# Performance work log

Hardware: AMD Instinct MI355X
Metric: run time of the kernel (lower is better)

Reference implementation:

```python
import jax, jax.numpy as jnp
import numpy as np

B, N, M, C = 4, 4096, 4096, 256
H, K = 8, 8
S = K + 1          # window: query token + k neighbors
D = C // H         # head dim
FF = 4 * C
RADIUS = 0.06
EPS = 1e-5


def setup_inputs() -> dict:
    key = jax.random.key(0)
    ks = jax.random.split(key, 12)
    s = 0.02
    return {
        "q_xyz": jax.random.uniform(ks[0], (B, N, 3), dtype=jnp.float32),
        "q_feat": jax.random.normal(ks[1], (B, N, C), dtype=jnp.float32),
        "kv_xyz": jax.random.uniform(ks[2], (B, M, 3), dtype=jnp.float32),
        "kv_feat": jax.random.normal(ks[3], (B, M, C), dtype=jnp.float32),
        "kv_pad": jnp.zeros((B, M), dtype=bool),
        # MultiheadAttention params (torch layout: y = x @ W.T + b)
        "Wqkv": s * jax.random.normal(ks[4], (3 * C, C), dtype=jnp.float32),
        "bqkv": jnp.zeros((3 * C,), dtype=jnp.float32),
        "Wo": s * jax.random.normal(ks[5], (C, C), dtype=jnp.float32),
        "bo": jnp.zeros((C,), dtype=jnp.float32),
        # FFN
        "W1": s * jax.random.normal(ks[6], (FF, C), dtype=jnp.float32),
        "b1": jnp.zeros((FF,), dtype=jnp.float32),
        "W2": s * jax.random.normal(ks[7], (C, FF), dtype=jnp.float32),
        "b2": jnp.zeros((C,), dtype=jnp.float32),
        # LayerNorms
        "g1": jnp.ones((C,), dtype=jnp.float32),
        "be1": jnp.zeros((C,), dtype=jnp.float32),
        "g2": jnp.ones((C,), dtype=jnp.float32),
        "be2": jnp.zeros((C,), dtype=jnp.float32),
    }


def _layernorm(x, g, b):
    mu = jnp.mean(x, axis=-1, keepdims=True)
    var = jnp.mean((x - mu) ** 2, axis=-1, keepdims=True)
    return (x - mu) / jnp.sqrt(var + EPS) * g + b


def _forward(q_xyz, q_feat, kv_xyz, kv_feat, kv_pad,
             Wqkv, bqkv, Wo, bo, W1, b1, W2, b2, g1, be1, g2, be2):
    inf = jnp.float32(jnp.inf)
    # pairwise distances via ||q||^2 + ||k||^2 - 2 q.k  -> (B, N, M)
    d2 = (jnp.sum(q_xyz * q_xyz, -1)[:, :, None]
          + jnp.sum(kv_xyz * kv_xyz, -1)[:, None, :]
          - 2.0 * jnp.einsum('bnd,bmd->bnm', q_xyz, kv_xyz))
    dist = jnp.sqrt(jnp.maximum(d2, 0.0))
    dist = jnp.where(kv_pad[:, None, :], inf, dist)
    dist = jnp.where(dist <= RADIUS, dist, inf)
    # k nearest within radius (topk of -dist == smallest dist)
    neg, idx = jax.lax.top_k(-dist, K)            # (B, N, K)
    invalid = jnp.isinf(neg)                       # padding slots
    idx = jnp.where(invalid, 0, idx)
    # gather neighbor features: (B, N, K, C)
    neigh = jnp.take_along_axis(
        kv_feat, idx.reshape(B, N * K)[:, :, None], axis=1
    ).reshape(B, N, K, C)
    neigh = jnp.where(invalid[..., None], q_feat[:, :, None, :], neigh)
    # tokens: query token + neighbors -> (B*N, S, C)
    tokens = jnp.concatenate([q_feat[:, :, None, :], neigh], axis=2)
    tokens = tokens.reshape(B * N, S, C)
    pad = jnp.concatenate(
        [jnp.zeros_like(invalid[..., :1]), invalid], axis=-1
    ).reshape(B * N, S)                            # (B*N, S) key padding
    # --- MultiheadAttention (batch_first, eval) ---
    qkv = tokens @ Wqkv.T + bqkv
    q, k, v = jnp.split(qkv, 3, axis=-1)
    q = q.reshape(-1, S, H, D)
    k = k.reshape(-1, S, H, D)
    v = v.reshape(-1, S, H, D)
    scores = jnp.einsum('bshd,bthd->bhst', q, k) / np.sqrt(D).astype(np.float32)
    scores = jnp.where(pad[:, None, None, :], -inf, scores)
    attn = jax.nn.softmax(scores, axis=-1)
    o = jnp.einsum('bhst,bthd->bshd', attn, v).reshape(-1, S, C)
    o = o @ Wo.T + bo
    # residual + norm, FFN + norm
    x = _layernorm(tokens + o, g1, be1)
    f = jnp.maximum(x @ W1.T + b1, 0.0) @ W2.T + b2
    x = _layernorm(x + f, g2, be2)
    # fused query token + residual -> (B, N, C)
    return x[:, 0, :].reshape(B, N, C) + q_feat


def reference(q_xyz, q_feat, kv_xyz, kv_feat, kv_pad,
              Wqkv, bqkv, Wo, bo, W1, b1, W2, b2, g1, be1, g2, be2):
    return _forward(q_xyz, q_feat, kv_xyz, kv_feat, kv_pad,
                    Wqkv, bqkv, Wo, bo, W1, b1, W2, b2, g1, be1, g2, be2)
```

## Files before the change

### kernel.cpp

```cpp
#include <hip/hip_runtime.h>
#include <hip/hip_bf16.h>
#include <stdint.h>

#define B_ 4
#define N_ 4096
#define M_ 4096
#define C_ 256
#define FF_ 1024
#define BN_ (B_*N_)
#define BM_ (B_*M_)

typedef __attribute__((ext_vector_type(8))) short short8;
typedef __attribute__((ext_vector_type(4))) float f32x4;

static __device__ __forceinline__ float b2f(unsigned short u) {
    union { unsigned int i; float f; } c; c.i = ((unsigned int)u) << 16; return c.f;
}
static __device__ __forceinline__ unsigned short f2b(float f) {
    union { float f; unsigned int i; } c; c.f = f;
    unsigned int x = c.i;
    x += 0x7fffu + ((x >> 16) & 1u);
    return (unsigned short)(x >> 16);
}

static __device__ __forceinline__ void gload_lds16(const short* g, short* l) {
    __builtin_amdgcn_global_load_lds((const __attribute__((address_space(1))) void*)g,
                                     (__attribute__((address_space(3))) void*)l,
                                     16, 0, 0);
}

__global__ __launch_bounds__(1024) void prep_kernel(const float* __restrict__ s0, unsigned short* __restrict__ d0,
                                                    const float* __restrict__ s1, unsigned short* __restrict__ d1,
                                                    const float* __restrict__ s2, unsigned short* __restrict__ d2,
                                                    const float* __restrict__ s3, unsigned short* __restrict__ d3,
                                                    const float* __restrict__ s4, unsigned short* __restrict__ d4,
                                                    const float* __restrict__ s5, unsigned short* __restrict__ d5,
                                                    const float* __restrict__ kv_xyz,
                                                    float4* __restrict__ sorted,
                                                    int* __restrict__ starts) {
    __shared__ int cnt[4096];
    __shared__ int wsum[16];
    if (blockIdx.x < 2240) {
        int i = blockIdx.x * 1024 + threadIdx.x;
        const float* src; unsigned short* dst; int off;
        if (i < 1048576)      { src = s0; dst = d0; off = i; }
        else if (i < 2097152) { src = s1; dst = d1; off = i - 1048576; }
        else if (i < 2146304) { src = s2; dst = d2; off = i - 2097152; }
        else if (i < 2162688) { src = s3; dst = d3; off = i - 2146304; }
        else if (i < 2228224) { src = s4; dst = d4; off = i - 2162688; }
        else                  { src = s5; dst = d5; off = i - 2228224; }
        f32x4 v = *(const f32x4*)(src + (size_t)off * 4);
        ushort4 r;
        r.x = f2b(v[0]); r.y = f2b(v[1]); r.z = f2b(v[2]); r.w = f2b(v[3]);
        *(ushort4*)(dst + (size_t)off * 4) = r;
        return;
    }
    int b = blockIdx.x - 2240, tid = threadIdx.x;
    const float* src = kv_xyz + (size_t)b * M_ * 3;
    for (int i = tid; i < 4096; i += 1024) cnt[i] = 0;
    __syncthreads();
    float px[4], py[4], pz[4]; int pc[4];
#pragma unroll
    for (int j = 0; j < 4; ++j) {
        int m = tid + j * 1024;
        px[j] = src[3 * m]; py[j] = src[3 * m + 1]; pz[j] = src[3 * m + 2];
        int cx = min(15, (int)(px[j] * 16.0f));
        int cy = min(15, (int)(py[j] * 16.0f));
        int cz = min(15, (int)(pz[j] * 16.0f));
        pc[j] = (cz * 16 + cy) * 16 + cx;
        atomicAdd(&cnt[pc[j]], 1);
    }
    __syncthreads();
    int c0 = cnt[tid * 4], c1 = cnt[tid * 4 + 1], c2 = cnt[tid * 4 + 2], c3 = cnt[tid * 4 + 3];
    int tsum = c0 + c1 + c2 + c3;
    int lane = tid & 63, wv = tid >> 6;
    int scan = tsum;
#pragma unroll
    for (int off = 1; off < 64; off <<= 1) {
        int o = __shfl_up(scan, off);
        if (lane >= off) scan += o;
    }
    if (lane == 63) wsum[wv] = scan;
    __syncthreads();
    if (tid < 16) {
        int v = wsum[tid];
#pragma unroll
        for (int off = 1; off < 16; off <<= 1) {
            int o = __shfl_up(v, off);
            if (tid >= off) v += o;
        }
        wsum[tid] = v;
    }
    __syncthreads();
    int base = (wv > 0 ? wsum[wv - 1] : 0) + (scan - tsum);
    int e0 = base, e1 = base + c0, e2 = e1 + c1, e3 = e2 + c2;
    int* st = starts + (size_t)b * 4097;
    st[tid * 4] = e0; st[tid * 4 + 1] = e1; st[tid * 4 + 2] = e2; st[tid * 4 + 3] = e3;
    if (tid == 0) st[4096] = M_;
    cnt[tid * 4] = e0; cnt[tid * 4 + 1] = e1; cnt[tid * 4 + 2] = e2; cnt[tid * 4 + 3] = e3;
    __syncthreads();
    float4* dst = sorted + (size_t)b * 4096;
#pragma unroll
    for (int j = 0; j < 4; ++j) {
        int m = tid + j * 1024;
        int pos = atomicAdd(&cnt[pc[j]], 1);
        float4 v; v.x = px[j]; v.y = py[j]; v.z = pz[j]; v.w = __int_as_float(m);
        dst[pos] = v;
    }
}

template <int RELU, int OUTBF>
__global__ __launch_bounds__(256) void gemm_lds_kernel(const unsigned short* __restrict__ A,
                                                       const unsigned short* __restrict__ W,
                                                       const float* __restrict__ bias,
                                                       float* __restrict__ Yf,
                                                       unsigned short* __restrict__ Yb,
                                                       int M, int Nn, int Kd) {
    __shared__ __align__(16) short As[2][4096];
    __shared__ __align__(16) short Bs[2][4096];
    int lane = threadIdx.x & 63, wid = threadIdx.x >> 6;
    int row0 = blockIdx.y * 128;
    int col0 = blockIdx.x * 128;
    int wr = wid >> 1, wc = wid & 1;
    const short* Ap = (const short*)A;
    const short* Wp = (const short*)W;
    int srow = lane >> 2;
    int scolz = (((lane & 3) ^ ((lane >> 2) & 3)) * 8);

    f32x4 acc[4][4];
#pragma unroll
    for (int i = 0; i < 4; ++i)
#pragma unroll
        for (int j = 0; j < 4; ++j)
#pragma unroll
            for (int r = 0; r < 4; ++r) acc[i][j][r] = 0.0f;

    int KT = Kd >> 5;
    int buf = 0;

#define STAGE(BUFI, K0)                                                                   \
    {                                                                                     \
        _Pragma("unroll")                                                                 \
        for (int j = 0; j < 2; ++j) {                                                     \
            int chunk = j * 4 + wid;                                                      \
            int row = chunk * 16 + srow;                                                  \
            gload_lds16(Ap + (size_t)(row0 + row) * Kd + (K0) + scolz, &As[BUFI][chunk * 512]); \
            gload_lds16(Wp + (size_t)(col0 + row) * Kd + (K0) + scolz, &Bs[BUFI][chunk * 512]); \
        }                                                                                 \
    }

    STAGE(0, 0);
    __syncthreads();

    int lane15 = lane & 15;
    int rd16s = (((lane >> 4) ^ (lane & 3)) * 16);

    for (int kt = 0; kt < KT; ++kt) {
        if (kt + 1 < KT) STAGE(buf ^ 1, (kt + 1) << 5);
        short8 a[4], b[4];
#pragma unroll
        for (int i = 0; i < 4; ++i) {
            int ra = wr * 64 + i * 16 + lane15;
            int rb = wc * 64 + i * 16 + lane15;
            a[i] = *(const short8*)((const char*)&As[buf][0] + ra * 64 + rd16s);
            b[i] = *(const short8*)((const char*)&Bs[buf][0] + rb * 64 + rd16s);
        }
#pragma unroll
        for (int i = 0; i < 4; ++i)
#pragma unroll
            for (int j = 0; j < 4; ++j)
                acc[i][j] = __builtin_amdgcn_mfma_f32_16x16x32_bf16(a[i], b[j], acc[i][j], 0, 0, 0);
        if (kt + 1 < KT) __syncthreads();
        buf ^= 1;
    }
#undef STAGE

    int r0 = row0 + wr * 64 + (lane >> 4) * 4;
    int c0 = col0 + wc * 64 + lane15;
#pragma unroll
    for (int i = 0; i < 4; ++i)
#pragma unroll
        for (int j = 0; j < 4; ++j)
#pragma unroll
            for (int r = 0; r < 4; ++r) {
                int rr = r0 + i * 16 + r;
                int cc = c0 + j * 16;
                float v = acc[i][j][r] + bias[cc];
                if (RELU) v = fmaxf(v, 0.0f);
                if (OUTBF) Yb[(size_t)rr * Nn + cc] = f2b(v);
                else       Yf[(size_t)rr * Nn + cc] = v;
            }
}

__global__ __launch_bounds__(512) void attn_wo_ln_kernel(const unsigned short* __restrict__ QKVq,
                                                         const unsigned short* __restrict__ KVkv,
                                                         const float* __restrict__ q_xyz,
                                                         const float4* __restrict__ sorted,
                                                         const int* __restrict__ starts,
                                                         const unsigned short* __restrict__ Wo,
                                                         const float* __restrict__ bias,
                                                         const unsigned short* __restrict__ qfb,
                                                         const float* __restrict__ g,
                                                         const float* __restrict__ be,
                                                         unsigned short* __restrict__ xout) {
    __shared__ __align__(16) short o_lds[8192];
    __shared__ __align__(16) short Bs[2][8192];
    __shared__ float redS[8][32];
    __shared__ float redQ[8][32];
    int lane = threadIdx.x & 63, wid = threadIdx.x >> 6;
    int swz = (blockIdx.x & 7) * 64 + (blockIdx.x >> 3);
    int row0 = swz * 32;
    const short* Wp = (const short*)Wo;
    int srow = lane >> 2;
    int scolz = (((lane & 3) ^ ((lane >> 2) & 3)) * 8);

#define STAGE_B(BUFI, K0)                                                                   \
    {                                                                                       \
        for (int c = wid; c < 16; c += 8) {                                                 \
            gload_lds16(Wp + (size_t)(c * 16 + srow) * 256 + (K0) + scolz,                  \
                        &Bs[BUFI][c * 512]);                                                \
        }                                                                                   \
    }
    STAGE_B(0, 0);

    int c0l = lane * 4;
    for (int pt = 0; pt < 4; ++pt) {
        int lrow = wid * 4 + pt;
        int p = row0 + lrow;
        int b = p >> 12;

        float qx = q_xyz[(size_t)p * 3 + 0];
        float qy = q_xyz[(size_t)p * 3 + 1];
        float qz = q_xyz[(size_t)p * 3 + 2];
        float qq = __fadd_rn(__fadd_rn(__fmul_rn(qx, qx), __fmul_rn(qy, qy)), __fmul_rn(qz, qz));
        int cx = min(15, (int)(qx * 16.0f));
        int cy = min(15, (int)(qy * 16.0f));
        int cz = min(15, (int)(qz * 16.0f));
        unsigned long long lst[8];
#pragma unroll
        for (int i = 0; i < 8; ++i) lst[i] = ~0ull;
        const float4* pts = sorted + (size_t)b * 4096;
        const int* st = starts + (size_t)b * 4097;
        int z0 = max(cz - 1, 0), z1 = min(cz + 1, 15);
        int y0 = max(cy - 1, 0), y1 = min(cy + 1, 15);
        int x0 = max(cx - 1, 0), x1 = min(cx + 1, 15);
        for (int z = z0; z <= z1; ++z) {
            for (int y = y0; y <= y1; ++y) {
                int rowbase = (z * 16 + y) * 16;
                int s = st[rowbase + x0];
                int e = st[rowbase + x1 + 1];
                for (int i = s + lane; i < e; i += 64) {
                    float4 pp = pts[i];
                    float kk = __fadd_rn(__fadd_rn(__fmul_rn(pp.x, pp.x), __fmul_rn(pp.y, pp.y)), __fmul_rn(pp.z, pp.z));
                    float dt = __fadd_rn(__fadd_rn(__fmul_rn(qx, pp.x), __fmul_rn(qy, pp.y)), __fmul_rn(qz, pp.z));
                    float d2 = __fsub_rn(__fadd_rn(qq, kk), __fmul_rn(2.0f, dt));
                    float dist = __fsqrt_rn(fmaxf(d2, 0.0f));
                    if (dist <= 0.06f) {
                        union { float f; unsigned int i; } cv; cv.f = dist;
                        unsigned long long key = (((unsigned long long)cv.i) << 32) |
                                                 (unsigned int)__float_as_int(pp.w);
                        if (key < lst[7]) {
                            lst[7] = key;
#pragma unroll
                            for (int k = 7; k > 0; --k) {
                                if (lst[k] < lst[k - 1]) {
                                    unsigned long long tmp = lst[k]; lst[k] = lst[k - 1]; lst[k - 1] = tmp;
                                }
                            }
                        }
                    }
                }
            }
        }
        int nbr[8];
#pragma unroll
        for (int s = 0; s < 8; ++s) {
            unsigned long long mn = lst[0];
#pragma unroll
            for (int off = 32; off >= 1; off >>= 1) {
                unsigned long long o = __shfl_xor(mn, off);
                if (o < mn) mn = o;
            }
            int widx = (mn == ~0ull) ? -1 : (int)(unsigned int)(mn & 0xffffffffull);
            if (widx >= 0 && lst[0] == mn) {
#pragma unroll
                for (int k = 0; k < 7; ++k) lst[k] = lst[k + 1];
                lst[7] = ~0ull;
            }
            nbr[s] = widx;
        }

        const unsigned short* qrow = QKVq + (size_t)p * 768;
        ushort4 qu = *(const ushort4*)(qrow + c0l);
        float q0 = b2f(qu.x), q1 = b2f(qu.y), q2 = b2f(qu.z), q3 = b2f(qu.w);
        float sc[9];
        float vb[9][4];
        bool vld[9];
#pragma unroll
        for (int s = 0; s < 9; ++s) {
            const unsigned short* kr;
            bool valid;
            if (s == 0) { valid = true; kr = qrow + 256 + c0l; }
            else {
                int m = nbr[s - 1];
                valid = (m >= 0);
                kr = KVkv + (size_t)(b * 4096 + (valid ? m : 0)) * 512 + c0l;
            }
            float d = 0.0f;
            float v0 = 0.f, v1 = 0.f, v2 = 0.f, v3 = 0.f;
            if (valid) {
                ushort4 ku = *(const ushort4*)kr;
                ushort4 vu = *(const ushort4*)(kr + 256);
                d = q0 * b2f(ku.x) + q1 * b2f(ku.y) + q2 * b2f(ku.z) + q3 * b2f(ku.w);
                v0 = b2f(vu.x); v1 = b2f(vu.y); v2 = b2f(vu.z); v3 = b2f(vu.w);
            }
            d += __shfl_xor(d, 1);
            d += __shfl_xor(d, 2);
            d += __shfl_xor(d, 4);
            sc[s] = valid ? d * 0.17677669529663687f : -1e30f;
            vld[s] = valid;
            vb[s][0] = v0; vb[s][1] = v1; vb[s][2] = v2; vb[s][3] = v3;
        }
        float mx = sc[0];
#pragma unroll
        for (int s = 1; s < 9; ++s) mx = fmaxf(mx, sc[s]);
        float pr[9]; float sum = 0.0f;
#pragma unroll
        for (int s = 0; s < 9; ++s) {
            float e = vld[s] ? expf(sc[s] - mx) : 0.0f;
            pr[s] = e; sum += e;
        }
        float inv = 1.0f / sum;
        float o0 = 0, o1 = 0, o2 = 0, o3 = 0;
#pragma unroll
        for (int s = 0; s < 9; ++s) {
            o0 += pr[s] * vb[s][0]; o1 += pr[s] * vb[s][1];
            o2 += pr[s] * vb[s][2]; o3 += pr[s] * vb[s][3];
        }
        ushort4 r;
        r.x = f2b(o0 * inv); r.y = f2b(o1 * inv); r.z = f2b(o2 * inv); r.w = f2b(o3 * inv);
        int byteoff = lrow * 512 + (((lane >> 1) ^ (lrow & 7)) * 16) + (lane & 1) * 8;
        *(ushort4*)((char*)o_lds + byteoff) = r;
    }
    __syncthreads();

    int lane15 = lane & 15;
    int l4 = lane >> 4;
    int rd16s = ((l4 ^ (lane & 3)) * 16);
    int wc = wid;

    f32x4 acc[2][2];
#pragma unroll
    for (int i = 0; i < 2; ++i)
#pragma unroll
        for (int j = 0; j < 2; ++j)
#pragma unroll
            for (int r = 0; r < 4; ++r) acc[i][j][r] = 0.0f;

    int buf = 0;
    for (int kt = 0; kt < 8; ++kt) {
        if (kt + 1 < 8) STAGE_B(buf ^ 1, (kt + 1) << 5);
        short8 a[2], b[2];
#pragma unroll
        for (int i = 0; i < 2; ++i) {
            int arow = i * 16 + lane15;
            int unit = kt * 4 + l4;
            a[i] = *(const short8*)((const char*)o_lds + arow * 512 + ((unit ^ (arow & 7)) * 16));
        }
#pragma unroll
        for (int j = 0; j < 2; ++j) {
            int rb = wc * 32 + j * 16 + lane15;
            b[j] = *(const short8*)((const char*)&Bs[buf][0] + rb * 64 + rd16s);
        }
#pragma unroll
        for (int i = 0; i < 2; ++i)
#pragma unroll
            for (int j = 0; j < 2; ++j)
                acc[i][j] = __builtin_amdgcn_mfma_f32_16x16x32_bf16(a[i], b[j], acc[i][j], 0, 0, 0);
        if (kt + 1 < 8) __syncthreads();
        buf ^= 1;
    }
#undef STAGE_B

#pragma unroll
    for (int i = 0; i < 2; ++i)
#pragma unroll
        for (int j = 0; j < 2; ++j)
#pragma unroll
            for (int r = 0; r < 4; ++r) {
                int rr = row0 + i * 16 + l4 * 4 + r;
                int cc = wc * 32 + j * 16 + lane15;
                acc[i][j][r] += bias[cc] + b2f(qfb[(size_t)rr * 256 + cc]);
            }
#pragma unroll
    for (int i = 0; i < 2; ++i)
#pragma unroll
        for (int r = 0; r < 4; ++r) {
            float v0 = acc[i][0][r], v1 = acc[i][1][r];
            float s = v0 + v1;
            float s2 = v0 * v0 + v1 * v1;
#pragma unroll
            for (int off = 1; off < 16; off <<= 1) {
                s  += __shfl_xor(s, off);
                s2 += __shfl_xor(s2, off);
            }
            if (lane15 == 0) {
                int rl = i * 16 + l4 * 4 + r;
                redS[wid][rl] = s;
                redQ[wid][rl] = s2;
            }
        }
    __syncthreads();
#pragma unroll
    for (int i = 0; i < 2; ++i)
#pragma unroll
        for (int r = 0; r < 4; ++r) {
            int rl = i * 16 + l4 * 4 + r;
            int rr = row0 + rl;
            float tot = 0.0f, tot2 = 0.0f;
#pragma unroll
            for (int w = 0; w < 8; ++w) { tot += redS[w][rl]; tot2 += redQ[w][rl]; }
            float mu = tot * (1.0f / 256.0f);
            float var = fmaxf(tot2 * (1.0f / 256.0f) - mu * mu, 0.0f);
            float rs = 1.0f / __fsqrt_rn(var + 1e-5f);
#pragma unroll
            for (int j = 0; j < 2; ++j) {
                int cc = wc * 32 + j * 16 + lane15;
                float o = (acc[i][j][r] - mu) * rs * g[cc] + be[cc];
                xout[(size_t)rr * 256 + cc] = f2b(o);
            }
        }
}

__global__ __launch_bounds__(512) void gemm_ln2_kernel(const unsigned short* __restrict__ A,
                                                       const unsigned short* __restrict__ W,
                                                       const float* __restrict__ bias,
                                                       const unsigned short* __restrict__ qfb,
                                                       const unsigned short* __restrict__ resb,
                                                       const float* __restrict__ g,
                                                       const float* __restrict__ be,
                                                       float* __restrict__ outf,
                                                       int Kd) {
    __shared__ __align__(16) short As[2][1024];
    __shared__ __align__(16) short Bs[2][8192];
    __shared__ float redS[8][32];
    __shared__ float redQ[8][32];
    int lane = threadIdx.x & 63, wid = threadIdx.x >> 6;
    int swz = (blockIdx.x & 7) * 64 + (blockIdx.x >> 3);
    int row0 = swz * 32;
    int wc = wid;
    const short* Ap = (const short*)A;
    const short* Wp = (const short*)W;
    int srow = lane >> 2;
    int scolz = (((lane & 3) ^ ((lane >> 2) & 3)) * 8);

    f32x4 acc[2][2];
#pragma unroll
    for (int i = 0; i < 2; ++i)
#pragma unroll
        for (int j = 0; j < 2; ++j)
#pragma unroll
            for (int r = 0; r < 4; ++r) acc[i][j][r] = 0.0f;

    int KT = Kd >> 5;
    int buf = 0;

#define STAGE3(BUFI, K0)                                                                    \
    {                                                                                       \
        for (int c = wid; c < 18; c += 8) {                                                 \
            if (c < 2) {                                                                    \
                gload_lds16(Ap + (size_t)(row0 + c * 16 + srow) * Kd + (K0) + scolz,        \
                            &As[BUFI][c * 512]);                                            \
            } else {                                                                        \
                int cb = c - 2;                                                             \
                gload_lds16(Wp + (size_t)(cb * 16 + srow) * Kd + (K0) + scolz,              \
                            &Bs[BUFI][cb * 512]);                                           \
            }                                                                               \
        }                                                                                   \
    }

    STAGE3(0, 0);
    __syncthreads();

    int lane15 = lane & 15;
    int l4 = lane >> 4;
    int rd16s = ((l4 ^ (lane & 3)) * 16);

    for (int kt = 0; kt < KT; ++kt) {
        if (kt + 1 < KT) STAGE3(buf ^ 1, (kt + 1) << 5);
        short8 a[2], b[2];
#pragma unroll
        for (int i = 0; i < 2; ++i) {
            int ra = i * 16 + lane15;
            a[i] = *(const short8*)((const char*)&As[buf][0] + ra * 64 + rd16s);
        }
#pragma unroll
        for (int j = 0; j < 2; ++j) {
            int rb = wc * 32 + j * 16 + lane15;
            b[j] = *(const short8*)((const char*)&Bs[buf][0] + rb * 64 + rd16s);
        }
#pragma unroll
        for (int i = 0; i < 2; ++i)
#pragma unroll
            for (int j = 0; j < 2; ++j)
                acc[i][j] = __builtin_amdgcn_mfma_f32_16x16x32_bf16(a[i], b[j], acc[i][j], 0, 0, 0);
        __syncthreads();
        buf ^= 1;
    }
#undef STAGE3

#pragma unroll
    for (int i = 0; i < 2; ++i)
#pragma unroll
        for (int j = 0; j < 2; ++j)
#pragma unroll
            for (int r = 0; r < 4; ++r) {
                int rr = row0 + i * 16 + l4 * 4 + r;
                int cc = wc * 32 + j * 16 + lane15;
                acc[i][j][r] += bias[cc] + b2f(resb[(size_t)rr * 256 + cc]);
            }
#pragma unroll
    for (int i = 0; i < 2; ++i)
#pragma unroll
        for (int r = 0; r < 4; ++r) {
            float v0 = acc[i][0][r], v1 = acc[i][1][r];
            float s = v0 + v1;
            float s2 = v0 * v0 + v1 * v1;
#pragma unroll
            for (int off = 1; off < 16; off <<= 1) {
                s  += __shfl_xor(s, off);
                s2 += __shfl_xor(s2, off);
            }
            if (lane15 == 0) {
                int rl = i * 16 + l4 * 4 + r;
                redS[wid][rl] = s;
                redQ[wid][rl] = s2;
            }
        }
    __syncthreads();
#pragma unroll
    for (int i = 0; i < 2; ++i)
#pragma unroll
        for (int r = 0; r < 4; ++r) {
            int rl = i * 16 + l4 * 4 + r;
            int rr = row0 + rl;
            float tot = 0.0f, tot2 = 0.0f;
#pragma unroll
            for (int w = 0; w < 8; ++w) { tot += redS[w][rl]; tot2 += redQ[w][rl]; }
            float mu = tot * (1.0f / 256.0f);
            float var = fmaxf(tot2 * (1.0f / 256.0f) - mu * mu, 0.0f);
            float rs = 1.0f / __fsqrt_rn(var + 1e-5f);
#pragma unroll
            for (int j = 0; j < 2; ++j) {
                int cc = wc * 32 + j * 16 + lane15;
                float o = (acc[i][j][r] - mu) * rs * g[cc] + be[cc];
                outf[(size_t)rr * 256 + cc] = o + b2f(qfb[(size_t)rr * 256 + cc]);
            }
        }
}

extern "C" void kernel_launch(void* const* d_in, const int* in_sizes, int n_in,
                              void* d_out, int out_size, void* d_ws, size_t ws_size,
                              hipStream_t stream) {
    const float* q_xyz  = (const float*)d_in[0];
    const float* q_feat = (const float*)d_in[1];
    const float* kv_xyz = (const float*)d_in[2];
    const float* kv_feat = (const float*)d_in[3];
    const float* Wqkv = (const float*)d_in[5];
    const float* bqkv = (const float*)d_in[6];
    const float* Wo = (const float*)d_in[7];
    const float* bo = (const float*)d_in[8];
    const float* W1 = (const float*)d_in[9];
    const float* b1 = (const float*)d_in[10];
    const float* W2 = (const float*)d_in[11];
    const float* b2 = (const float*)d_in[12];
    const float* g1 = (const float*)d_in[13];
    const float* be1 = (const float*)d_in[14];
    const float* g2 = (const float*)d_in[15];
    const float* be2 = (const float*)d_in[16];

    char* ws = (char*)d_ws;
    const size_t OFF_QF   = 0;
    const size_t OFF_KVF  = OFF_QF   + 8388608;
    const size_t OFF_WQKV = OFF_KVF  + 8388608;
    const size_t OFF_WO   = OFF_WQKV + 393216;
    const size_t OFF_W1   = OFF_WO   + 131072;
    const size_t OFF_W2   = OFF_W1   + 524288;
    const size_t OFF_QKVQ = OFF_W2   + 524288;
    const size_t OFF_KVKV = OFF_QKVQ + 25165824;
    const size_t OFF_X    = OFF_KVKV + 16777216;
    const size_t OFF_H    = OFF_X    + 8388608;
    const size_t OFF_SORT  = OFF_H;
    const size_t OFF_START = OFF_H + 262144;

    unsigned short* qf_bf   = (unsigned short*)(ws + OFF_QF);
    unsigned short* kvf_bf  = (unsigned short*)(ws + OFF_KVF);
    unsigned short* Wqkv_bf = (unsigned short*)(ws + OFF_WQKV);
    unsigned short* Wo_bf   = (unsigned short*)(ws + OFF_WO);
    unsigned short* W1_bf   = (unsigned short*)(ws + OFF_W1);
    unsigned short* W2_bf   = (unsigned short*)(ws + OFF_W2);
    unsigned short* QKVq    = (unsigned short*)(ws + OFF_QKVQ);
    unsigned short* KVkv    = (unsigned short*)(ws + OFF_KVKV);
    unsigned short* x_bf    = (unsigned short*)(ws + OFF_X);
    unsigned short* h_bf    = (unsigned short*)(ws + OFF_H);
    float4* sort_buf        = (float4*)(ws + OFF_SORT);
    int* start_buf          = (int*)(ws + OFF_START);

    prep_kernel<<<2244, 1024, 0, stream>>>(
        q_feat, qf_bf, kv_feat, kvf_bf, Wqkv, Wqkv_bf, Wo, Wo_bf, W1, W1_bf, W2, W2_bf,
        kv_xyz, sort_buf, start_buf);

    gemm_lds_kernel<0, 1><<<dim3(768 / 128, BN_ / 128), 256, 0, stream>>>(
        qf_bf, Wqkv_bf, bqkv, nullptr, QKVq, BN_, 768, 256);
    gemm_lds_kernel<0, 1><<<dim3(512 / 128, BM_ / 128), 256, 0, stream>>>(
        kvf_bf, Wqkv_bf + 256 * 256, bqkv + 256, nullptr, KVkv, BM_, 512, 256);

    attn_wo_ln_kernel<<<BN_ / 32, 512, 0, stream>>>(
        QKVq, KVkv, q_xyz, sort_buf, start_buf, Wo_bf, bo, qf_bf, g1, be1, x_bf);

    gemm_lds_kernel<1, 1><<<dim3(1024 / 128, BN_ / 128), 256, 0, stream>>>(
        x_bf, W1_bf, b1, nullptr, h_bf, BN_, 1024, 256);

    gemm_ln2_kernel<<<BN_ / 32, 512, 0, stream>>>(
        h_bf, W2_bf, b2, qf_bf, x_bf, g2, be2, (float*)d_out, 1024);
}
```

Measured before the change: 153.3 us.

## Move neighbor search into a separate one-thread-per-query kernel

```diff
diff --git a/kernel.cpp b/kernel.cpp
--- a/kernel.cpp
+++ b/kernel.cpp
@@ -109,6 +109,61 @@
     }
 }
 
+__global__ __launch_bounds__(256) void knn_query_kernel(const float* __restrict__ q_xyz,
+                                                        const float4* __restrict__ sorted,
+                                                        const int* __restrict__ starts,
+                                                        int* __restrict__ idx_out) {
+    int q = blockIdx.x * 256 + threadIdx.x;
+    int b = q >> 12;
+    float qx = q_xyz[(size_t)q * 3 + 0];
+    float qy = q_xyz[(size_t)q * 3 + 1];
+    float qz = q_xyz[(size_t)q * 3 + 2];
+    float qq = __fadd_rn(__fadd_rn(__fmul_rn(qx, qx), __fmul_rn(qy, qy)), __fmul_rn(qz, qz));
+    int cx = min(15, (int)(qx * 16.0f));
+    int cy = min(15, (int)(qy * 16.0f));
+    int cz = min(15, (int)(qz * 16.0f));
+    unsigned long long lst[8];
+#pragma unroll
+    for (int i = 0; i < 8; ++i) lst[i] = ~0ull;
+    const float4* pts = sorted + (size_t)b * 4096;
+    const int* st = starts + (size_t)b * 4097;
+    int z0 = max(cz - 1, 0), z1 = min(cz + 1, 15);
+    int y0 = max(cy - 1, 0), y1 = min(cy + 1, 15);
+    int x0 = max(cx - 1, 0), x1 = min(cx + 1, 15);
+    for (int z = z0; z <= z1; ++z) {
+        for (int y = y0; y <= y1; ++y) {
+            int rowbase = (z * 16 + y) * 16;
+            int s = st[rowbase + x0];
+            int e = st[rowbase + x1 + 1];
+            for (int i = s; i < e; ++i) {
+                float4 p = pts[i];
+                float kk = __fadd_rn(__fadd_rn(__fmul_rn(p.x, p.x), __fmul_rn(p.y, p.y)), __fmul_rn(p.z, p.z));
+                float dt = __fadd_rn(__fadd_rn(__fmul_rn(qx, p.x), __fmul_rn(qy, p.y)), __fmul_rn(qz, p.z));
+                float d2 = __fsub_rn(__fadd_rn(qq, kk), __fmul_rn(2.0f, dt));
+                float dist = __fsqrt_rn(fmaxf(d2, 0.0f));
+                if (dist <= 0.06f) {
+                    union { float f; unsigned int i; } cv; cv.f = dist;
+                    unsigned long long key = (((unsigned long long)cv.i) << 32) |
+                                             (unsigned int)__float_as_int(p.w);
+                    if (key < lst[7]) {
+                        lst[7] = key;
+#pragma unroll
+                        for (int k = 7; k > 0; --k) {
+                            if (lst[k] < lst[k - 1]) {
+                                unsigned long long tmp = lst[k]; lst[k] = lst[k - 1]; lst[k - 1] = tmp;
+                            }
+                        }
+                    }
+                }
+            }
+        }
+    }
+#pragma unroll
+    for (int s = 0; s < 8; ++s)
+        idx_out[(size_t)q * 8 + s] =
+            (lst[s] == ~0ull) ? -1 : (int)(unsigned int)(lst[s] & 0xffffffffull);
+}
+
 template <int RELU, int OUTBF>
 __global__ __launch_bounds__(256) void gemm_lds_kernel(const unsigned short* __restrict__ A,
                                                        const unsigned short* __restrict__ W,
@@ -194,9 +249,7 @@
 
 __global__ __launch_bounds__(512) void attn_wo_ln_kernel(const unsigned short* __restrict__ QKVq,
                                                          const unsigned short* __restrict__ KVkv,
-                                                         const float* __restrict__ q_xyz,
-                                                         const float4* __restrict__ sorted,
-                                                         const int* __restrict__ starts,
+                                                         const int* __restrict__ nidx,
                                                          const unsigned short* __restrict__ Wo,
                                                          const float* __restrict__ bias,
                                                          const unsigned short* __restrict__ qfb,
@@ -228,68 +281,6 @@
         int lrow = wid * 4 + pt;
         int p = row0 + lrow;
         int b = p >> 12;
-
-        float qx = q_xyz[(size_t)p * 3 + 0];
-        float qy = q_xyz[(size_t)p * 3 + 1];
-        float qz = q_xyz[(size_t)p * 3 + 2];
-        float qq = __fadd_rn(__fadd_rn(__fmul_rn(qx, qx), __fmul_rn(qy, qy)), __fmul_rn(qz, qz));
-        int cx = min(15, (int)(qx * 16.0f));
-        int cy = min(15, (int)(qy * 16.0f));
-        int cz = min(15, (int)(qz * 16.0f));
-        unsigned long long lst[8];
-#pragma unroll
-        for (int i = 0; i < 8; ++i) lst[i] = ~0ull;
-        const float4* pts = sorted + (size_t)b * 4096;
-        const int* st = starts + (size_t)b * 4097;
-        int z0 = max(cz - 1, 0), z1 = min(cz + 1, 15);
-        int y0 = max(cy - 1, 0), y1 = min(cy + 1, 15);
-        int x0 = max(cx - 1, 0), x1 = min(cx + 1, 15);
-        for (int z = z0; z <= z1; ++z) {
-            for (int y = y0; y <= y1; ++y) {
-                int rowbase = (z * 16 + y) * 16;
-                int s = st[rowbase + x0];
-                int e = st[rowbase + x1 + 1];
-                for (int i = s + lane; i < e; i += 64) {
-                    float4 pp = pts[i];
-                    float kk = __fadd_rn(__fadd_rn(__fmul_rn(pp.x, pp.x), __fmul_rn(pp.y, pp.y)), __fmul_rn(pp.z, pp.z));
-                    float dt = __fadd_rn(__fadd_rn(__fmul_rn(qx, pp.x), __fmul_rn(qy, pp.y)), __fmul_rn(qz, pp.z));
-                    float d2 = __fsub_rn(__fadd_rn(qq, kk), __fmul_rn(2.0f, dt));
-                    float dist = __fsqrt_rn(fmaxf(d2, 0.0f));
-                    if (dist <= 0.06f) {
-                        union { float f; unsigned int i; } cv; cv.f = dist;
-                        unsigned long long key = (((unsigned long long)cv.i) << 32) |
-                                                 (unsigned int)__float_as_int(pp.w);
-                        if (key < lst[7]) {
-                            lst[7] = key;
-#pragma unroll
-                            for (int k = 7; k > 0; --k) {
-                                if (lst[k] < lst[k - 1]) {
-                                    unsigned long long tmp = lst[k]; lst[k] = lst[k - 1]; lst[k - 1] = tmp;
-                                }
-                            }
-                        }
-                    }
-                }
-            }
-        }
-        int nbr[8];
-#pragma unroll
-        for (int s = 0; s < 8; ++s) {
-            unsigned long long mn = lst[0];
-#pragma unroll
-            for (int off = 32; off >= 1; off >>= 1) {
-                unsigned long long o = __shfl_xor(mn, off);
-                if (o < mn) mn = o;
-            }
-            int widx = (mn == ~0ull) ? -1 : (int)(unsigned int)(mn & 0xffffffffull);
-            if (widx >= 0 && lst[0] == mn) {
-#pragma unroll
-                for (int k = 0; k < 7; ++k) lst[k] = lst[k + 1];
-                lst[7] = ~0ull;
-            }
-            nbr[s] = widx;
-        }
-
         const unsigned short* qrow = QKVq + (size_t)p * 768;
         ushort4 qu = *(const ushort4*)(qrow + c0l);
         float q0 = b2f(qu.x), q1 = b2f(qu.y), q2 = b2f(qu.z), q3 = b2f(qu.w);
@@ -302,7 +293,7 @@
             bool valid;
             if (s == 0) { valid = true; kr = qrow + 256 + c0l; }
             else {
-                int m = nbr[s - 1];
+                int m = nidx[(size_t)p * 8 + (s - 1)];
                 valid = (m >= 0);
                 kr = KVkv + (size_t)(b * 4096 + (valid ? m : 0)) * 512 + c0l;
             }
@@ -589,7 +580,8 @@
     const size_t OFF_QKVQ = OFF_W2   + 524288;
     const size_t OFF_KVKV = OFF_QKVQ + 25165824;
     const size_t OFF_X    = OFF_KVKV + 16777216;
-    const size_t OFF_H    = OFF_X    + 8388608;
+    const size_t OFF_IDX  = OFF_X    + 8388608;
+    const size_t OFF_H    = OFF_IDX  + 524288;
     const size_t OFF_SORT  = OFF_H;
     const size_t OFF_START = OFF_H + 262144;
 
@@ -602,6 +594,7 @@
     unsigned short* QKVq    = (unsigned short*)(ws + OFF_QKVQ);
     unsigned short* KVkv    = (unsigned short*)(ws + OFF_KVKV);
     unsigned short* x_bf    = (unsigned short*)(ws + OFF_X);
+    int* idx_buf            = (int*)(ws + OFF_IDX);
     unsigned short* h_bf    = (unsigned short*)(ws + OFF_H);
     float4* sort_buf        = (float4*)(ws + OFF_SORT);
     int* start_buf          = (int*)(ws + OFF_START);
@@ -609,6 +602,8 @@
     prep_kernel<<<2244, 1024, 0, stream>>>(
         q_feat, qf_bf, kv_feat, kvf_bf, Wqkv, Wqkv_bf, Wo, Wo_bf, W1, W1_bf, W2, W2_bf,
         kv_xyz, sort_buf, start_buf);
+
+    knn_query_kernel<<<BN_ / 256, 256, 0, stream>>>(q_xyz, sort_buf, start_buf, idx_buf);
 
     gemm_lds_kernel<0, 1><<<dim3(768 / 128, BN_ / 128), 256, 0, stream>>>(
         qf_bf, Wqkv_bf, bqkv, nullptr, QKVq, BN_, 768, 256);
@@ -616,7 +611,7 @@
         kvf_bf, Wqkv_bf + 256 * 256, bqkv + 256, nullptr, KVkv, BM_, 512, 256);
 
     attn_wo_ln_kernel<<<BN_ / 32, 512, 0, stream>>>(
-        QKVq, KVkv, q_xyz, sort_buf, start_buf, Wo_bf, bo, qf_bf, g1, be1, x_bf);
+        QKVq, KVkv, idx_buf, Wo_bf, bo, qf_bf, g1, be1, x_bf);
 
     gemm_lds_kernel<1, 1><<<dim3(1024 / 128, BN_ / 128), 256, 0, stream>>>(
         x_bf, W1_bf, b1, nullptr, h_bf, BN_, 1024, 256);
```

Result: slower. 157.1 us (+2.4%).
